# Optimization experiments

Hardware: AMD Instinct MI355X
Metric: run time of the kernel (lower is better)

## Reference

```python
import jax, jax.numpy as jnp
import numpy as np

EPS = 1e-8
BN_EPS = 1e-5


def _gelu(x):
    return jax.nn.gelu(x, approximate=False)


def _batchnorm(x, gamma, beta):
    # PyTorch BatchNorm1d training-mode: biased variance over the batch dim
    mean = jnp.mean(x, axis=0)
    var = jnp.mean((x - mean) ** 2, axis=0)
    return (x - mean) * jax.lax.rsqrt(var + BN_EPS) * gamma + beta


def setup_inputs() -> dict:
    key = jax.random.key(0)
    N, E, K = 100000, 1600000, 4
    H = 64  # hidden_dim; edge MLP 8 -> H -> H//2 -> H//4
    ks = jax.random.split(key, 16)
    inp = {
        "coords": jax.random.normal(ks[0], (N, 3), jnp.float32),
        "normals": jax.random.normal(ks[1], (N, 3), jnp.float32),
        "curvatures": jax.random.normal(ks[2], (N, K), jnp.float32),
        "edge_index": jax.random.randint(ks[3], (2, E), 0, N, jnp.int64),
        "W1": jax.random.normal(ks[4], (8, H), jnp.float32) * (1.0 / np.sqrt(8)),
        "b1": jnp.zeros((H,), jnp.float32),
        "W2": jax.random.normal(ks[5], (H, H // 2), jnp.float32) * (1.0 / np.sqrt(H)),
        "b2": jnp.zeros((H // 2,), jnp.float32),
        "W3": jax.random.normal(ks[6], (H // 2, H // 4), jnp.float32) * (1.0 / np.sqrt(H // 2)),
        "b3": jnp.zeros((H // 4,), jnp.float32),
        "bn_e_gamma": jnp.ones((H // 4,), jnp.float32),
        "bn_e_beta": jnp.zeros((H // 4,), jnp.float32),
        "Wp": jax.random.normal(ks[7], (H // 4, H // 4), jnp.float32) * (1.0 / np.sqrt(H // 4)),
        "bp": jnp.zeros((H // 4,), jnp.float32),
        "bn_n_gamma": jnp.ones((H // 4,), jnp.float32),
        "bn_n_beta": jnp.zeros((H // 4,), jnp.float32),
    }
    return inp


def reference(coords, normals, curvatures, edge_index,
              W1, b1, W2, b2, W3, b3, bn_e_gamma, bn_e_beta,
              Wp, bp, bn_n_gamma, bn_n_beta):
    N = coords.shape[0]
    D = W3.shape[1]  # hidden_dim // 4
    row, col = edge_index[0], edge_index[1]

    # gather endpoint features per edge
    delta = coords[col] - coords[row]                                   # [E,3]
    n_row, n_col = normals[row], normals[col]
    normal_dot = jnp.sum(n_row * n_col, axis=-1, keepdims=True)         # [E,1]
    dnorm = jnp.linalg.norm(delta, axis=-1, keepdims=True) + EPS
    cos_r = jnp.clip(jnp.sum(n_row * delta, axis=-1, keepdims=True) / dnorm, -1 + EPS, 1 - EPS)
    cos_c = jnp.clip(jnp.sum(n_col * delta, axis=-1, keepdims=True) / dnorm, -1 + EPS, 1 - EPS)
    curv_diff = curvatures[col, :2] - curvatures[row, :2]               # [E,2]
    ef_raw = jnp.concatenate([delta, normal_dot, cos_r, cos_c, curv_diff], axis=-1)  # [E,8]

    # small edge MLP
    h = _gelu(ef_raw @ W1 + b1)
    h = _gelu(h @ W2 + b2)
    ef = h @ W3 + b3                                                    # [E,D]
    ef = _batchnorm(ef, bn_e_gamma, bn_e_beta)

    # scatter edge features to both endpoints with degree normalization
    node_feat = jnp.zeros((N, D), ef.dtype).at[row].add(ef).at[col].add(ef)
    ones = jnp.ones(row.shape, ef.dtype)
    degree = jnp.zeros((N,), ef.dtype).at[row].add(ones).at[col].add(ones)
    degree = jnp.maximum(degree, 1.0)
    node_feat = node_feat / degree[:, None]

    node_feat = node_feat @ Wp + bp
    node_feat = _batchnorm(node_feat, bn_n_gamma, bn_n_beta)
    return node_feat
```

## Files before the change

kernel.cpp:

```cpp
#include <hip/hip_runtime.h>
#include <hip/hip_fp16.h>
#include <math.h>

#define WG 256

typedef _Float16 f16x8 __attribute__((ext_vector_type(8)));
typedef float    f32x4 __attribute__((ext_vector_type(4)));

__device__ __forceinline__ float gelu_f(float x) {
    float u = 0.7978845608028654f * x * fmaf(0.044715f * x, x, 1.0f);
    u = fminf(fmaxf(u, -9.0f), 9.0f);
    const float e = __expf(2.0f * u);
    return 0.5f * x * (1.0f + __fdividef(e - 1.0f, e + 1.0f));
}

__device__ __forceinline__ __half2 gelu2(float xa, float xb) {
    float ua = 0.7978845608f * xa * fmaf(0.044715f * xa, xa, 1.0f);
    float ub = 0.7978845608f * xb * fmaf(0.044715f * xb, xb, 1.0f);
    ua = fminf(fmaxf(ua, -4.2f), 4.2f);
    ub = fminf(fmaxf(ub, -4.2f), 4.2f);
    const __half2 e   = h2exp(__float22half2_rn(make_float2(2.0f * ua, 2.0f * ub)));
    const __half2 one = __float2half2_rn(1.0f);
    const __half2 t   = __hmul2(__hsub2(e, one), h2rcp(__hadd2(e, one)));
    const float2  tf  = __half22float2(t);
    return __float22half2_rn(make_float2(0.5f * xa * (1.0f + tf.x),
                                         0.5f * xb * (1.0f + tf.y)));
}

#define WAVE_LDS_FENCE() asm volatile("s_waitcnt lgkmcnt(0)" ::: "memory")

__device__ __forceinline__ void acc_h4(f32x4& s, uint2 r) {
    const __half2 ha = *(const __half2*)&r.x;
    const __half2 hb = *(const __half2*)&r.y;
    const float2 fa = __half22float2(ha);
    const float2 fb = __half22float2(hb);
    s[0] += fa.x; s[1] += fa.y; s[2] += fb.x; s[3] += fb.y;
}

__global__ __launch_bounds__(WG, 4) void edge_mlp_mfma(
    const float* __restrict__ coords,
    const float* __restrict__ normals,
    const float* __restrict__ curv,
    const int*   __restrict__ eidx,
    const float* __restrict__ W1, const float* __restrict__ b1,
    const float* __restrict__ W2, const float* __restrict__ b2,
    const float* __restrict__ W3, const float* __restrict__ b3,
    __half* __restrict__ ef16, int* __restrict__ cnt,
    int* __restrict__ slots, _Float16* __restrict__ ellA,
    int es, int mode,
    float* __restrict__ stats, int E)
{
    __shared__ __half h1s[4][32][68];
    __shared__ __half h2s[4][32][36];
    __shared__ float red[4][32];

    const int t    = threadIdx.x;
    const int w    = t >> 6;
    const int lane = t & 63;
    const int quad = lane >> 4;
    const int col  = lane & 15;

    const int e  = blockIdx.x * WG + w * 64 + lane;
    const bool ev = (e < E);
    const int ec = ev ? e : 0;
    const int r = eidx[ec];
    const int c = eidx[E + ec];

    int pr = 0, qc = 0;
    if (ev) {
        pr = atomicAdd(&cnt[r], 1);
        qc = atomicAdd(&cnt[c], 1);
    }
    const int packR = (ev && pr < es) ? r * es + pr : -1;
    const int packC = (ev && qc < es) ? c * es + qc : -1;

    f16x8 bw1[4];
#pragma unroll
    for (int n = 0; n < 4; ++n) {
#pragma unroll
        for (int j = 0; j < 8; ++j) {
            const int k = quad * 8 + j;
            bw1[n][j] = (k < 8) ? (_Float16)W1[k * 64 + n * 16 + col] : (_Float16)0.f;
        }
    }
    f16x8 bw2[2][2];
#pragma unroll
    for (int s = 0; s < 2; ++s)
#pragma unroll
        for (int n = 0; n < 2; ++n)
#pragma unroll
            for (int j = 0; j < 8; ++j)
                bw2[s][n][j] = (_Float16)W2[(s * 32 + quad * 8 + j) * 32 + n * 16 + col];
    f16x8 bw3;
#pragma unroll
    for (int j = 0; j < 8; ++j)
        bw3[j] = (_Float16)W3[(quad * 8 + j) * 16 + col];

    float b1v[4], b2v[2], b3v;
#pragma unroll
    for (int n = 0; n < 4; ++n) b1v[n] = b1[n * 16 + col];
    b2v[0] = b2[col]; b2v[1] = b2[16 + col];
    b3v = b3[col];

    const float rx = coords[3*r], ry = coords[3*r+1], rz = coords[3*r+2];
    const float cx = coords[3*c], cy = coords[3*c+1], cz = coords[3*c+2];
    const float dx = cx - rx, dy = cy - ry, dz = cz - rz;
    const float nrx = normals[3*r], nry = normals[3*r+1], nrz = normals[3*r+2];
    const float ncx = normals[3*c], ncy = normals[3*c+1], ncz = normals[3*c+2];

    const float ndot = nrx*ncx + nry*ncy + nrz*ncz;
    const float dn   = sqrtf(dx*dx + dy*dy + dz*dz) + 1e-8f;
    const float inv  = 1.0f / dn;
    const float lo = -1.0f + 1e-8f, hi = 1.0f - 1e-8f;
    const float cr = fminf(fmaxf((nrx*dx + nry*dy + nrz*dz) * inv, lo), hi);
    const float cc2 = fminf(fmaxf((ncx*dx + ncy*dy + ncz*dz) * inv, lo), hi);
    const float cd0 = curv[4*c]   - curv[4*r];
    const float cd1 = curv[4*c+1] - curv[4*r+1];

    float f[8] = {dx, dy, dz, ndot, cr, cc2, cd0, cd1};

    if (mode == 1 && ev) {
        if (pr < es) slots[(size_t)r * es + pr] = e;
        if (qc < es) slots[(size_t)c * es + qc] = e;
    }

    const int e0w = blockIdx.x * WG + w * 64;
    float vsum = 0.f, vsq = 0.f;

#pragma unroll
    for (int p = 0; p < 2; ++p) {
#pragma unroll
        for (int mtl = 0; mtl < 2; ++mtl) {
            const int mt = 2 * p + mtl;
            f16x8 a1;
#pragma unroll
            for (int j = 0; j < 8; ++j) {
                const float v = __shfl(f[j], (mt << 4) + col, 64);
                a1[j] = (quad == 0) ? (_Float16)v : (_Float16)0.f;
            }
            f32x4 c1[4];
#pragma unroll
            for (int n = 0; n < 4; ++n) {
                f32x4 c0 = {b1v[n], b1v[n], b1v[n], b1v[n]};
                c1[n] = __builtin_amdgcn_mfma_f32_16x16x32_f16(a1, bw1[n], c0, 0, 0, 0);
            }
#pragma unroll
            for (int np = 0; np < 2; ++np)
#pragma unroll
                for (int rg = 0; rg < 4; ++rg) {
                    const __half2 g = gelu2(c1[2*np][rg], c1[2*np+1][rg]);
                    __half* dst = &h1s[w][mtl*16 + quad*4 + rg][np*32 + col];
                    dst[0]  = __low2half(g);
                    dst[16] = __high2half(g);
                }
        }
        WAVE_LDS_FENCE();

        f32x4 c2s[2][2];
#pragma unroll
        for (int mtl = 0; mtl < 2; ++mtl) {
            const f16x8 a2s0 = *(const f16x8*)&h1s[w][mtl*16 + col][quad * 8];
            const f16x8 a2s1 = *(const f16x8*)&h1s[w][mtl*16 + col][32 + quad * 8];
#pragma unroll
            for (int n = 0; n < 2; ++n) {
                f32x4 c0 = {b2v[n], b2v[n], b2v[n], b2v[n]};
                c0 = __builtin_amdgcn_mfma_f32_16x16x32_f16(a2s0, bw2[0][n], c0, 0, 0, 0);
                c2s[mtl][n] = __builtin_amdgcn_mfma_f32_16x16x32_f16(a2s1, bw2[1][n], c0, 0, 0, 0);
            }
        }
#pragma unroll
        for (int mtl = 0; mtl < 2; ++mtl)
#pragma unroll
            for (int rg = 0; rg < 4; ++rg) {
                const __half2 g = gelu2(c2s[mtl][0][rg], c2s[mtl][1][rg]);
                __half* dst = &h2s[w][mtl*16 + quad*4 + rg][col];
                dst[0]  = __low2half(g);
                dst[16] = __high2half(g);
            }
        WAVE_LDS_FENCE();

#pragma unroll
        for (int mtl = 0; mtl < 2; ++mtl) {
            const int mt = 2 * p + mtl;
            const f16x8 a3 = *(const f16x8*)&h2s[w][mtl*16 + col][quad * 8];
            f32x4 c0 = {b3v, b3v, b3v, b3v};
            const f32x4 c3 = __builtin_amdgcn_mfma_f32_16x16x32_f16(a3, bw3, c0, 0, 0, 0);

#pragma unroll
            for (int rg = 0; rg < 4; ++rg) {
                const int me = e0w + mt * 16 + quad * 4 + rg;
                if (me < E) { vsum += c3[rg]; vsq += c3[rg] * c3[rg]; }
            }

            if (mode == 2) {
#pragma unroll
                for (int rg = 0; rg < 4; ++rg)
                    h1s[w][mtl*16 + quad*4 + rg][col] = __float2half(c3[rg]);
            } else {
#pragma unroll
                for (int rg = 0; rg < 4; ++rg) {
                    const int me = e0w + mt * 16 + quad * 4 + rg;
                    if (me < E) ef16[(size_t)me * 16 + col] = __float2half(c3[rg]);
                }
            }
        }

        if (mode == 2) {
            WAVE_LDS_FENCE();
            const int j    = lane >> 2;
            const int subl = lane & 3;
#pragma unroll
            for (int mtl = 0; mtl < 2; ++mtl) {
                const int mt = 2 * p + mtl;
                const uint2 v = *(const uint2*)&h1s[w][mtl*16 + j][subl * 4];
                const int srcl = (mt << 4) + j;
                const int dR = __shfl(packR, srcl, 64);
                const int dC = __shfl(packC, srcl, 64);
                if (dR >= 0) *(uint2*)((char*)ellA + (size_t)dR * 32 + subl * 8) = v;
                if (dC >= 0) *(uint2*)((char*)ellA + (size_t)dC * 32 + subl * 8) = v;
            }
        }
    }

    vsum += __shfl_xor(vsum, 16, 64);
    vsq  += __shfl_xor(vsq,  16, 64);
    vsum += __shfl_xor(vsum, 32, 64);
    vsq  += __shfl_xor(vsq,  32, 64);
    if (lane < 16) {
        red[w][col]      = vsum;
        red[w][16 + col] = vsq;
    }
    __syncthreads();
    if (t < 32) {
        const float s = red[0][t] + red[1][t] + red[2][t] + red[3][t];
        atomicAdd(&stats[t], s);
    }
}

__global__ __launch_bounds__(WG) void gather_seq_kernel(
    const _Float16* __restrict__ ellA, const int* __restrict__ cnt,
    const float* __restrict__ Wp, const float* __restrict__ bp,
    const float* __restrict__ gE, const float* __restrict__ bE,
    float* __restrict__ stats, float* __restrict__ X,
    int N, float invE, int es)
{
    __shared__ float sWp[256];
    __shared__ f32x4 syv[4][16][4];
    __shared__ float red2[4][32];

    const int t = threadIdx.x;
    sWp[t] = Wp[t];

    const int w    = t >> 6;
    const int lane = t & 63;
    const int g    = lane >> 2;
    const int subl = lane & 3;
    const int c0   = subl * 4;

    float a[4], bb[4], bpv[4];
#pragma unroll
    for (int cc = 0; cc < 4; ++cc) {
        const int ch = c0 + cc;
        const float mean = stats[ch] * invE;
        const float var  = stats[16 + ch] * invE - mean * mean;
        a[cc]  = gE[ch] * rsqrtf(var + 1e-5f);
        bb[cc] = bE[ch] - mean * a[cc];
        bpv[cc] = bp[ch];
    }

    const int node = blockIdx.x * 64 + w * 16 + g;

    f32x4 s = {0.f, 0.f, 0.f, 0.f};
    int len = 0;
    if (node < N) {
        len = cnt[node];
        const int cap = len < es ? len : es;
        const char* base = (const char*)ellA + (size_t)node * es * 32 + subl * 8;
        int i = 0;
        for (; i + 4 <= cap; i += 4) {
            const uint2 r0 = *(const uint2*)(base + (size_t)(i    ) * 32);
            const uint2 r1 = *(const uint2*)(base + (size_t)(i + 1) * 32);
            const uint2 r2 = *(const uint2*)(base + (size_t)(i + 2) * 32);
            const uint2 r3 = *(const uint2*)(base + (size_t)(i + 3) * 32);
            acc_h4(s, r0); acc_h4(s, r1); acc_h4(s, r2); acc_h4(s, r3);
        }
        for (; i < cap; ++i) {
            const uint2 r0 = *(const uint2*)(base + (size_t)i * 32);
            acc_h4(s, r0);
        }
    }

    const float d    = (float)len;
    const float invd = 1.0f / fmaxf(d, 1.0f);
    f32x4 y;
#pragma unroll
    for (int cc = 0; cc < 4; ++cc)
        y[cc] = (a[cc] * s[cc] + bb[cc] * d) * invd;

    syv[w][g][subl] = y;
    __syncthreads();

    const f32x4 y0 = syv[w][g][0];
    const f32x4 y1 = syv[w][g][1];
    const f32x4 y2 = syv[w][g][2];
    const f32x4 y3 = syv[w][g][3];

    const f32x4* sWp4 = (const f32x4*)sWp;
    f32x4 x = {bpv[0], bpv[1], bpv[2], bpv[3]};
#pragma unroll
    for (int j = 0; j < 4; ++j) {
        const f32x4 wj = sWp4[j * 4 + subl];
#pragma unroll
        for (int cc = 0; cc < 4; ++cc) x[cc] += y0[j] * wj[cc];
    }
#pragma unroll
    for (int j = 0; j < 4; ++j) {
        const f32x4 wj = sWp4[(4 + j) * 4 + subl];
#pragma unroll
        for (int cc = 0; cc < 4; ++cc) x[cc] += y1[j] * wj[cc];
    }
#pragma unroll
    for (int j = 0; j < 4; ++j) {
        const f32x4 wj = sWp4[(8 + j) * 4 + subl];
#pragma unroll
        for (int cc = 0; cc < 4; ++cc) x[cc] += y2[j] * wj[cc];
    }
#pragma unroll
    for (int j = 0; j < 4; ++j) {
        const f32x4 wj = sWp4[(12 + j) * 4 + subl];
#pragma unroll
        for (int cc = 0; cc < 4; ++cc) x[cc] += y3[j] * wj[cc];
    }

    if (node < N) {
        *(f32x4*)&X[(size_t)node * 16 + c0] = x;
    } else {
        x = (f32x4){0.f, 0.f, 0.f, 0.f};
    }

    f32x4 vs = x, vq;
#pragma unroll
    for (int cc = 0; cc < 4; ++cc) vq[cc] = x[cc] * x[cc];
#pragma unroll
    for (int off = 4; off <= 32; off <<= 1) {
#pragma unroll
        for (int cc = 0; cc < 4; ++cc) {
            vs[cc] += __shfl_xor(vs[cc], off, 64);
            vq[cc] += __shfl_xor(vq[cc], off, 64);
        }
    }
    if (lane < 4) {
#pragma unroll
        for (int cc = 0; cc < 4; ++cc) {
            red2[w][c0 + cc]      = vs[cc];
            red2[w][16 + c0 + cc] = vq[cc];
        }
    }
    __syncthreads();
    if (t < 32) {
        const float ssum = red2[0][t] + red2[1][t] + red2[2][t] + red2[3][t];
        atomicAdd(&stats[32 + t], ssum);
    }
}

__global__ __launch_bounds__(WG) void scan_blocks_kernel(
    const int* __restrict__ cnt, int* __restrict__ rowptr,
    int* __restrict__ bsum, int N)
{
    __shared__ int sd[WG];
    const int t = threadIdx.x;
    const int i = blockIdx.x * WG + t;
    const int v = (i < N) ? cnt[i] : 0;
    sd[t] = v;
    __syncthreads();
    for (int off = 1; off < WG; off <<= 1) {
        int x = 0;
        if (t >= off) x = sd[t - off];
        __syncthreads();
        sd[t] += x;
        __syncthreads();
    }
    if (i < N) rowptr[i] = sd[t] - v;
    if (t == WG - 1) bsum[blockIdx.x] = sd[t];
}

__global__ __launch_bounds__(512) void scan_top_kernel(
    const int* __restrict__ bsum, int* __restrict__ boff, int nblk)
{
    __shared__ int sd[512];
    const int t = threadIdx.x;
    const int v = (t < nblk) ? bsum[t] : 0;
    sd[t] = v;
    __syncthreads();
    for (int off = 1; off < 512; off <<= 1) {
        int x = 0;
        if (t >= off) x = sd[t - off];
        __syncthreads();
        sd[t] += x;
        __syncthreads();
    }
    if (t < nblk) boff[t] = sd[t] - v;
}

__global__ __launch_bounds__(WG) void scan_add_kernel(
    int* __restrict__ rowptr, int* __restrict__ cursor,
    const int* __restrict__ boff, int N)
{
    const int i = blockIdx.x * WG + threadIdx.x;
    if (i < N) {
        const int v = rowptr[i] + boff[blockIdx.x];
        rowptr[i] = v;
        cursor[i] = v;
    }
}

__global__ __launch_bounds__(WG) void build_kernel(
    const int* __restrict__ eidx, int* __restrict__ cursor,
    int* __restrict__ slots, int E)
{
    const int e = blockIdx.x * WG + threadIdx.x;
    if (e < E) {
        const int r = eidx[e];
        const int c = eidx[E + e];
        const int p = atomicAdd(&cursor[r], 1);
        slots[p] = e;
        const int q = atomicAdd(&cursor[c], 1);
        slots[q] = e;
    }
}

__global__ __launch_bounds__(WG) void gather_kernel(
    const __half* __restrict__ ef16, const int* __restrict__ slots,
    const int* __restrict__ rowptr, const int* __restrict__ cnt,
    const float* __restrict__ Wp, const float* __restrict__ bp,
    const float* __restrict__ gE, const float* __restrict__ bE,
    float* __restrict__ stats, float* __restrict__ X,
    int N, float invE, int es)
{
    __shared__ float sWp[256];
    __shared__ f32x4 syv[4][16][4];
    __shared__ float red2[4][32];

    const int t = threadIdx.x;
    sWp[t] = Wp[t];

    const int w    = t >> 6;
    const int lane = t & 63;
    const int g    = lane >> 2;
    const int subl = lane & 3;
    const int c0   = subl * 4;

    float a[4], bb[4], bpv[4];
#pragma unroll
    for (int cc = 0; cc < 4; ++cc) {
        const int ch = c0 + cc;
        const float mean = stats[ch] * invE;
        const float var  = stats[16 + ch] * invE - mean * mean;
        a[cc]  = gE[ch] * rsqrtf(var + 1e-5f);
        bb[cc] = bE[ch] - mean * a[cc];
        bpv[cc] = bp[ch];
    }

    const int node = blockIdx.x * 64 + w * 16 + g;

    f32x4 s = {0.f, 0.f, 0.f, 0.f};
    int len = 0;
    if (node < N) {
        len = cnt[node];
        const size_t base = (es > 0) ? (size_t)node * (size_t)es : (size_t)rowptr[node];
        const int cap = (es > 0) ? (len < es ? len : es) : len;
        const int* sl = slots + base;
        int i = 0;
        for (; i + 4 <= cap; i += 4) {
            const int e0 = sl[i], e1 = sl[i+1], e2 = sl[i+2], e3 = sl[i+3];
            const uint2 r0 = *(const uint2*)(ef16 + (size_t)e0 * 16 + c0);
            const uint2 r1 = *(const uint2*)(ef16 + (size_t)e1 * 16 + c0);
            const uint2 r2 = *(const uint2*)(ef16 + (size_t)e2 * 16 + c0);
            const uint2 r3 = *(const uint2*)(ef16 + (size_t)e3 * 16 + c0);
            acc_h4(s, r0); acc_h4(s, r1); acc_h4(s, r2); acc_h4(s, r3);
        }
        for (; i < cap; ++i) {
            const uint2 r0 = *(const uint2*)(ef16 + (size_t)sl[i] * 16 + c0);
            acc_h4(s, r0);
        }
    }

    const float d    = (float)len;
    const float invd = 1.0f / fmaxf(d, 1.0f);
    f32x4 y;
#pragma unroll
    for (int cc = 0; cc < 4; ++cc)
        y[cc] = (a[cc] * s[cc] + bb[cc] * d) * invd;

    syv[w][g][subl] = y;
    __syncthreads();

    const f32x4 y0 = syv[w][g][0];
    const f32x4 y1 = syv[w][g][1];
    const f32x4 y2 = syv[w][g][2];
    const f32x4 y3 = syv[w][g][3];

    const f32x4* sWp4 = (const f32x4*)sWp;
    f32x4 x = {bpv[0], bpv[1], bpv[2], bpv[3]};
#pragma unroll
    for (int j = 0; j < 4; ++j) {
        const f32x4 wj = sWp4[j * 4 + subl];
#pragma unroll
        for (int cc = 0; cc < 4; ++cc) x[cc] += y0[j] * wj[cc];
    }
#pragma unroll
    for (int j = 0; j < 4; ++j) {
        const f32x4 wj = sWp4[(4 + j) * 4 + subl];
#pragma unroll
        for (int cc = 0; cc < 4; ++cc) x[cc] += y1[j] * wj[cc];
    }
#pragma unroll
    for (int j = 0; j < 4; ++j) {
        const f32x4 wj = sWp4[(8 + j) * 4 + subl];
#pragma unroll
        for (int cc = 0; cc < 4; ++cc) x[cc] += y2[j] * wj[cc];
    }
#pragma unroll
    for (int j = 0; j < 4; ++j) {
        const f32x4 wj = sWp4[(12 + j) * 4 + subl];
#pragma unroll
        for (int cc = 0; cc < 4; ++cc) x[cc] += y3[j] * wj[cc];
    }

    if (node < N) {
        *(f32x4*)&X[(size_t)node * 16 + c0] = x;
    } else {
        x = (f32x4){0.f, 0.f, 0.f, 0.f};
    }

    f32x4 vs = x, vq;
#pragma unroll
    for (int cc = 0; cc < 4; ++cc) vq[cc] = x[cc] * x[cc];
#pragma unroll
    for (int off = 4; off <= 32; off <<= 1) {
#pragma unroll
        for (int cc = 0; cc < 4; ++cc) {
            vs[cc] += __shfl_xor(vs[cc], off, 64);
            vq[cc] += __shfl_xor(vq[cc], off, 64);
        }
    }
    if (lane < 4) {
#pragma unroll
        for (int cc = 0; cc < 4; ++cc) {
            red2[w][c0 + cc]      = vs[cc];
            red2[w][16 + c0 + cc] = vq[cc];
        }
    }
    __syncthreads();
    if (t < 32) {
        const float ssum = red2[0][t] + red2[1][t] + red2[2][t] + red2[3][t];
        atomicAdd(&stats[32 + t], ssum);
    }
}

__global__ __launch_bounds__(WG) void out_kernel(
    const float* __restrict__ X, const float* __restrict__ stats,
    const float* __restrict__ gN, const float* __restrict__ bN,
    float* __restrict__ out, int total, float invN)
{
    __shared__ float sA[16], sB[16];
    if (threadIdx.x < 16) {
        const int k = threadIdx.x;
        const float mean = stats[32 + k] * invN;
        const float var  = stats[48 + k] * invN - mean * mean;
        const float a    = gN[k] / sqrtf(var + 1e-5f);
        sA[k] = a;
        sB[k] = bN[k] - mean * a;
    }
    __syncthreads();
    const int i = blockIdx.x * WG + threadIdx.x;
    if (i < total) {
        out[i] = sA[i & 15] * X[i] + sB[i & 15];
    }
}


extern "C" void kernel_launch(void* const* d_in, const int* in_sizes, int n_in,
                              void* d_out, int out_size, void* d_ws, size_t ws_size,
                              hipStream_t stream)
{
    const float* coords  = (const float*)d_in[0];
    const float* normals = (const float*)d_in[1];
    const float* curv    = (const float*)d_in[2];
    const int*   eidx    = (const int*)d_in[3];
    const float* W1 = (const float*)d_in[4];
    const float* b1 = (const float*)d_in[5];
    const float* W2 = (const float*)d_in[6];
    const float* b2 = (const float*)d_in[7];
    const float* W3 = (const float*)d_in[8];
    const float* b3 = (const float*)d_in[9];
    const float* gE = (const float*)d_in[10];
    const float* bE = (const float*)d_in[11];
    const float* Wp = (const float*)d_in[12];
    const float* bp = (const float*)d_in[13];
    const float* gN = (const float*)d_in[14];
    const float* bN = (const float*)d_in[15];

    const int N = in_sizes[0] / 3;
    const int E = in_sizes[3] / 2;
    const int eblk = (E + WG - 1) / WG;
    const int nblk = (N + WG - 1) / WG;
    float* out = (float*)d_out;

    const size_t off_cnt   = 256;
    const size_t cnt_bytes = (((size_t)N * 4) + 255) & ~(size_t)255;
    const size_t ef_bytes  = (size_t)E * 32;

    {
        const int es = 64;
        const size_t need_so = off_cnt + cnt_bytes + (size_t)N * (size_t)es * 32;
        if (ws_size >= need_so) {
            float*    stats = (float*)d_ws;
            int*      cnt   = (int*)((char*)d_ws + off_cnt);
            _Float16* ellA  = (_Float16*)((char*)d_ws + off_cnt + cnt_bytes);

            hipMemsetAsync(d_ws, 0, off_cnt + (size_t)N * 4, stream);

            edge_mlp_mfma<<<dim3(eblk), dim3(WG), 0, stream>>>(
                coords, normals, curv, eidx, W1, b1, W2, b2, W3, b3,
                (__half*)nullptr, cnt, (int*)nullptr, ellA, es, 2, stats, E);

            gather_seq_kernel<<<dim3((N + 63) / 64), dim3(WG), 0, stream>>>(
                ellA, cnt, Wp, bp, gE, bE, stats, out, N, 1.0f / (float)E, es);

            out_kernel<<<dim3((N * 16 + WG - 1) / WG), dim3(WG), 0, stream>>>(
                out, stats, gN, bN, out, N * 16, 1.0f / (float)N);
            return;
        }
    }

    {
        const size_t off_slots = off_cnt + cnt_bytes;
        int es = 0;
        const int strides[3] = {96, 80, 64};
        for (int si = 0; si < 3; ++si) {
            const size_t need = off_slots + (size_t)N * (size_t)strides[si] * 4 + ef_bytes;
            if (need <= ws_size) { es = strides[si]; break; }
        }
        if (es > 0) {
            float*  stats = (float*)d_ws;
            int*    cnt   = (int*)((char*)d_ws + off_cnt);
            int*    slots = (int*)((char*)d_ws + off_slots);
            __half* ef16  = (__half*)((char*)d_ws + off_slots + (size_t)N * (size_t)es * 4);

            hipMemsetAsync(d_ws, 0, off_cnt + (size_t)N * 4, stream);

            edge_mlp_mfma<<<dim3(eblk), dim3(WG), 0, stream>>>(
                coords, normals, curv, eidx, W1, b1, W2, b2, W3, b3,
                ef16, cnt, slots, (_Float16*)nullptr, es, 1, stats, E);

            gather_kernel<<<dim3((N + 63) / 64), dim3(WG), 0, stream>>>(
                ef16, slots, cnt, cnt, Wp, bp, gE, bE, stats, out,
                N, 1.0f / (float)E, es);

            out_kernel<<<dim3((N * 16 + WG - 1) / WG), dim3(WG), 0, stream>>>(
                out, stats, gN, bN, out, N * 16, 1.0f / (float)N);
            return;
        }
    }

    const size_t need_csr = (size_t)(64 + 3 * (size_t)N + 8192 + 2 * (size_t)E) * 4
                          + ef_bytes + 256;
    if (ws_size >= need_csr && nblk <= 4096) {
        float*  stats  = (float*)d_ws;
        int*    cnt    = (int*)(stats + 64);
        int*    rowptr = cnt + N;
        int*    cursor = rowptr + N;
        int*    bsum   = cursor + N;
        int*    boff   = bsum + 4096;
        int*    slots  = boff + 4096;
        __half* ef16   = (__half*)(slots + 2 * (size_t)E);

        hipMemsetAsync(d_ws, 0, (size_t)(64 + N) * 4, stream);

        edge_mlp_mfma<<<dim3(eblk), dim3(WG), 0, stream>>>(
            coords, normals, curv, eidx, W1, b1, W2, b2, W3, b3,
            ef16, cnt, slots, (_Float16*)nullptr, 0, 0, stats, E);

        scan_blocks_kernel<<<dim3(nblk), dim3(WG), 0, stream>>>(cnt, rowptr, bsum, N);
        scan_top_kernel<<<dim3(1), dim3(512), 0, stream>>>(bsum, boff, nblk);
        scan_add_kernel<<<dim3(nblk), dim3(WG), 0, stream>>>(rowptr, cursor, boff, N);
        build_kernel<<<dim3(eblk), dim3(WG), 0, stream>>>(eidx, cursor, slots, E);

        gather_kernel<<<dim3((N + 63) / 64), dim3(WG), 0, stream>>>(
            ef16, slots, rowptr, cnt, Wp, bp, gE, bE, stats, out,
            N, 1.0f / (float)E, 0);

        out_kernel<<<dim3((N * 16 + WG - 1) / WG), dim3(WG), 0, stream>>>(
            out, stats, gN, bN, out, N * 16, 1.0f / (float)N);
        return;
    }
}
```

Measured before the change: 371.7 us.

## Pack half2 LDS stores with permuted weights and widen ELL gather loads

The edge MLP now writes GELU outputs as packed half2 stores to LDS instead of two scalar half stores. To keep the math the same, the K index of the W2 and W3 B-operand fragments is permuted to match the interleaved column order. Occupancy launch bounds rise from 4 to 6 waves. The node kernel reads each ELL row pair with 16-byte loads split across lane pairs and combines the partial sums with xor shuffles, so it issues fewer, wider memory transactions. The tradeoff is the register pressure implied by the higher launch bound.

```diff
diff --git a/kernel.cpp b/kernel.cpp
--- a/kernel.cpp
+++ b/kernel.cpp
@@ -37,7 +37,9 @@
     s[0] += fa.x; s[1] += fa.y; s[2] += fb.x; s[3] += fb.y;
 }
 
-__global__ __launch_bounds__(WG, 4) void edge_mlp_mfma(
+__device__ __forceinline__ int permf(int q) { return (q >> 1) + ((q & 1) << 4); }
+
+__global__ __launch_bounds__(WG, 6) void edge_mlp_mfma(
     const float* __restrict__ coords,
     const float* __restrict__ normals,
     const float* __restrict__ curv,
@@ -89,12 +91,16 @@
 #pragma unroll
         for (int n = 0; n < 2; ++n)
 #pragma unroll
-            for (int j = 0; j < 8; ++j)
-                bw2[s][n][j] = (_Float16)W2[(s * 32 + quad * 8 + j) * 32 + n * 16 + col];
+            for (int j = 0; j < 8; ++j) {
+                const int q = quad * 8 + j;
+                bw2[s][n][j] = (_Float16)W2[(s * 32 + permf(q)) * 32 + n * 16 + col];
+            }
     f16x8 bw3;
 #pragma unroll
-    for (int j = 0; j < 8; ++j)
-        bw3[j] = (_Float16)W3[(quad * 8 + j) * 16 + col];
+    for (int j = 0; j < 8; ++j) {
+        const int q = quad * 8 + j;
+        bw3[j] = (_Float16)W3[permf(q) * 16 + col];
+    }
 
     float b1v[4], b2v[2], b3v;
 #pragma unroll
@@ -149,9 +155,7 @@
 #pragma unroll
                 for (int rg = 0; rg < 4; ++rg) {
                     const __half2 g = gelu2(c1[2*np][rg], c1[2*np+1][rg]);
-                    __half* dst = &h1s[w][mtl*16 + quad*4 + rg][np*32 + col];
-                    dst[0]  = __low2half(g);
-                    dst[16] = __high2half(g);
+                    *(__half2*)&h1s[w][mtl*16 + quad*4 + rg][np*32 + 2*col] = g;
                 }
         }
         WAVE_LDS_FENCE();
@@ -173,9 +177,7 @@
 #pragma unroll
             for (int rg = 0; rg < 4; ++rg) {
                 const __half2 g = gelu2(c2s[mtl][0][rg], c2s[mtl][1][rg]);
-                __half* dst = &h2s[w][mtl*16 + quad*4 + rg][col];
-                dst[0]  = __low2half(g);
-                dst[16] = __high2half(g);
+                *(__half2*)&h2s[w][mtl*16 + quad*4 + rg][2*col] = g;
             }
         WAVE_LDS_FENCE();
 
@@ -256,48 +258,60 @@
     const int g    = lane >> 2;
     const int subl = lane & 3;
     const int c0   = subl * 4;
-
-    float a[4], bb[4], bpv[4];
-#pragma unroll
-    for (int cc = 0; cc < 4; ++cc) {
-        const int ch = c0 + cc;
+    const int h0   = (subl & 1) * 8;
+
+    float a8[8], b8[8];
+#pragma unroll
+    for (int cc = 0; cc < 8; ++cc) {
+        const int ch = h0 + cc;
         const float mean = stats[ch] * invE;
         const float var  = stats[16 + ch] * invE - mean * mean;
-        a[cc]  = gE[ch] * rsqrtf(var + 1e-5f);
-        bb[cc] = bE[ch] - mean * a[cc];
-        bpv[cc] = bp[ch];
-    }
+        a8[cc] = gE[ch] * rsqrtf(var + 1e-5f);
+        b8[cc] = bE[ch] - mean * a8[cc];
+    }
+    float bpv[4];
+#pragma unroll
+    for (int cc = 0; cc < 4; ++cc) bpv[cc] = bp[c0 + cc];
 
     const int node = blockIdx.x * 64 + w * 16 + g;
 
-    f32x4 s = {0.f, 0.f, 0.f, 0.f};
+    f32x4 sA = {0.f,0.f,0.f,0.f}, sB = {0.f,0.f,0.f,0.f};
     int len = 0;
     if (node < N) {
         len = cnt[node];
         const int cap = len < es ? len : es;
-        const char* base = (const char*)ellA + (size_t)node * es * 32 + subl * 8;
+        const char* nb = (const char*)ellA + (size_t)node * es * 32;
         int i = 0;
-        for (; i + 4 <= cap; i += 4) {
-            const uint2 r0 = *(const uint2*)(base + (size_t)(i    ) * 32);
-            const uint2 r1 = *(const uint2*)(base + (size_t)(i + 1) * 32);
-            const uint2 r2 = *(const uint2*)(base + (size_t)(i + 2) * 32);
-            const uint2 r3 = *(const uint2*)(base + (size_t)(i + 3) * 32);
-            acc_h4(s, r0); acc_h4(s, r1); acc_h4(s, r2); acc_h4(s, r3);
-        }
-        for (; i < cap; ++i) {
-            const uint2 r0 = *(const uint2*)(base + (size_t)i * 32);
-            acc_h4(s, r0);
-        }
+        for (; i + 2 <= cap; i += 2) {
+            const uint4 rr = *(const uint4*)(nb + (size_t)i * 32 + subl * 16);
+            acc_h4(sA, make_uint2(rr.x, rr.y));
+            acc_h4(sB, make_uint2(rr.z, rr.w));
+        }
+        if (i < cap && subl < 2) {
+            const uint4 rr = *(const uint4*)(nb + (size_t)i * 32 + subl * 16);
+            acc_h4(sA, make_uint2(rr.x, rr.y));
+            acc_h4(sB, make_uint2(rr.z, rr.w));
+        }
+    }
+#pragma unroll
+    for (int cc = 0; cc < 4; ++cc) {
+        sA[cc] += __shfl_xor(sA[cc], 2, 64);
+        sB[cc] += __shfl_xor(sB[cc], 2, 64);
     }
 
     const float d    = (float)len;
     const float invd = 1.0f / fmaxf(d, 1.0f);
-    f32x4 y;
-#pragma unroll
-    for (int cc = 0; cc < 4; ++cc)
-        y[cc] = (a[cc] * s[cc] + bb[cc] * d) * invd;
-
-    syv[w][g][subl] = y;
+    f32x4 yA, yB;
+#pragma unroll
+    for (int cc = 0; cc < 4; ++cc) {
+        yA[cc] = (a8[cc]     * sA[cc] + b8[cc]     * d) * invd;
+        yB[cc] = (a8[4 + cc] * sB[cc] + b8[4 + cc] * d) * invd;
+    }
+
+    if (subl < 2) {
+        syv[w][g][(subl & 1) * 2]     = yA;
+        syv[w][g][(subl & 1) * 2 + 1] = yB;
+    }
     __syncthreads();
 
     const f32x4 y0 = syv[w][g][0];
```

Result: slower. 671.9 us (+80.8%).
